# Performance work log

Hardware: AMD Instinct MI355X
Metric: run time of the kernel (lower is better)

Reference implementation:

```python
import jax, jax.numpy as jnp
import numpy as np

N = 1024      # num_nodes
D = 64        # node_embedding_dim
H = 64        # hidden_dim
LN_EPS = 1e-5


def setup_inputs() -> dict:
    key = jax.random.key(0)
    ks = jax.random.split(key, 6)
    node_embeddings = jax.random.normal(ks[0], (N, D), dtype=jnp.float32)
    valid_mask = jax.random.randint(ks[1], (N * N,), 0, 2).astype(jnp.float32)
    s1 = 1.0 / np.sqrt(2 * D)
    s2 = 1.0 / np.sqrt(H)
    W1 = jax.random.normal(ks[2], (2 * D, H), dtype=jnp.float32) * s1
    b1 = jnp.zeros((H,), jnp.float32)
    g1 = jnp.ones((H,), jnp.float32)
    be1 = jnp.zeros((H,), jnp.float32)
    W2 = jax.random.normal(ks[3], (H, H), dtype=jnp.float32) * s2
    b2 = jnp.zeros((H,), jnp.float32)
    g2 = jnp.ones((H,), jnp.float32)
    be2 = jnp.zeros((H,), jnp.float32)
    W3 = jax.random.normal(ks[4], (H, 1), dtype=jnp.float32) * s2
    b3 = jnp.zeros((1,), jnp.float32)
    return {
        "node_embeddings": node_embeddings, "valid_mask": valid_mask,
        "W1": W1, "b1": b1, "g1": g1, "be1": be1,
        "W2": W2, "b2": b2, "g2": g2, "be2": be2,
        "W3": W3, "b3": b3,
    }


def _layer_norm(x, g, b):
    m = jnp.mean(x, axis=-1, keepdims=True)
    v = jnp.mean((x - m) ** 2, axis=-1, keepdims=True)
    return (x - m) * jax.lax.rsqrt(v + LN_EPS) * g + b


def reference(node_embeddings, valid_mask, W1, b1, g1, be1, W2, b2, g2, be2, W3, b3):
    n, d = node_embeddings.shape
    # Build all ordered pairs (i, j): concat([emb_i, emb_j]) -> [n*n, 2d]
    src = jnp.broadcast_to(node_embeddings[:, None, :], (n, n, d))
    tgt = jnp.broadcast_to(node_embeddings[None, :, :], (n, n, d))
    e = jnp.concatenate([src, tgt], axis=-1).reshape(n * n, 2 * d)
    # MLP: Linear -> LayerNorm -> ReLU (x2 hidden) -> Linear(1)
    h = jax.nn.relu(_layer_norm(e @ W1 + b1, g1, be1))
    h = jax.nn.relu(_layer_norm(h @ W2 + b2, g2, be2))
    scores = (h @ W3 + b3)[:, 0]  # [n*n]
    # Original never scores self-edges (i == j) and multiplies by valid_mask.
    off_diag = 1.0 - jnp.eye(n, dtype=scores.dtype).reshape(-1)
    return scores * valid_mask * off_diag
```

## Files before the change

kernel.cpp:

```cpp
#include <hip/hip_runtime.h>
#include <hip/hip_bf16.h>

#define NN 1024
#define LN_EPS 1e-5f

typedef __bf16 bf16x8 __attribute__((ext_vector_type(8)));
typedef float floatx4 __attribute__((ext_vector_type(4)));
typedef float floatx2 __attribute__((ext_vector_type(2)));

__global__ void precompute_ab(const float* __restrict__ emb, const float* __restrict__ W1,
                              const float* __restrict__ b1, const float* __restrict__ W2,
                              float* __restrict__ Ap, float* __restrict__ Bt,
                              float* __restrict__ sumA, float* __restrict__ sumB,
                              __bf16* __restrict__ Wf) {
    if (blockIdx.x == 1024) {
        int lane = threadIdx.x;
        int m_l = lane & 15, kg = lane >> 4;
#pragma unroll
        for (int mt = 0; mt < 4; mt++)
#pragma unroll
            for (int kc = 0; kc < 2; kc++) {
                bf16x8 f;
#pragma unroll
                for (int t = 0; t < 8; t++) {
                    int k = kc * 32 + kg * 8 + t;
                    f[t] = (__bf16)W2[k * 64 + mt * 16 + m_l];
                }
                *(bf16x8*)&Wf[((mt * 2 + kc) * 64 + lane) * 8] = f;
            }
        return;
    }
    __shared__ __align__(16) float e[64];
    int i = blockIdx.x, h = threadIdx.x;
    e[h] = emb[i * 64 + h];
    __syncthreads();
    float a = b1[h], b = 0.f;
#pragma unroll
    for (int d = 0; d < 64; d++) {
        a = fmaf(e[d], W1[d * 64 + h], a);
        b = fmaf(e[d], W1[(64 + d) * 64 + h], b);
    }
    Ap[i * 64 + h] = a;
    Bt[h * NN + i] = b;
    float ra = a, rb = b;
#pragma unroll
    for (int off = 1; off < 64; off <<= 1) {
        ra += __shfl_xor(ra, off);
        rb += __shfl_xor(rb, off);
    }
    if (h == 0) { sumA[i] = ra; sumB[i] = rb; }
}

__global__ __launch_bounds__(256, 4) void fused(
    const float* __restrict__ Ap, const float* __restrict__ Bt, const __bf16* __restrict__ Wf,
    const float* __restrict__ sumA, const float* __restrict__ sumB,
    const float* __restrict__ g1, const float* __restrict__ be1, const float* __restrict__ b2,
    const float* __restrict__ g2, const float* __restrict__ be2, const float* __restrict__ W3,
    const float* __restrict__ b3, const float* __restrict__ mask, float* __restrict__ out) {
    __shared__ __align__(16) __bf16 h1t[4][64 * 64];

    int tid = threadIdx.x;
    int wave = tid >> 6, lane = tid & 63;
    int i = blockIdx.x >> 2;
    int j0 = (blockIdx.x & 3) * 256 + wave * 64;

    int m_l = lane & 15, kg = lane >> 4;
    const float* Arow = Ap + i * 64;

    float sBj = sumB[j0 + lane];
    const float* btp = Bt + j0 + lane;
    floatx2 x2[32];
    floatx2 qa = {0.f, 0.f}, qb = {0.f, 0.f};
#pragma unroll
    for (int h2 = 0; h2 < 32; h2++) {
        floatx2 bb = { btp[(2 * h2) * NN], btp[(2 * h2 + 1) * NN] };
        floatx2 aa = *(const floatx2*)&Arow[2 * h2];
        floatx2 v = aa + bb;
        x2[h2] = v;
        if (h2 & 1) qb += v * v;
        else        qa += v * v;
    }
    floatx2 qs = qa + qb;
    float sq = qs[0] + qs[1];
    float m1 = (sumA[i] + sBj) * 0.015625f;
    float rs1 = rsqrtf(fmaf(m1, -m1, sq * 0.015625f) + LN_EPS);
    floatx2 p1 = {rs1, rs1};
    float ofs = -m1 * rs1;
    floatx2 o1 = {ofs, ofs};

    bf16x8 afrag[4][2];
#pragma unroll
    for (int mt = 0; mt < 4; mt++)
#pragma unroll
        for (int kc = 0; kc < 2; kc++)
            afrag[mt][kc] = *(const bf16x8*)&Wf[((mt * 2 + kc) * 64 + lane) * 8];

    __bf16* rowp = &h1t[wave][lane * 64];
    int sw = lane & 7;
#pragma unroll
    for (int c = 0; c < 8; c++) {
        bf16x8 fr;
#pragma unroll
        for (int t = 0; t < 4; t++) {
            floatx2 gg = *(const floatx2*)&g1[c * 8 + 2 * t];
            floatx2 ee = *(const floatx2*)&be1[c * 8 + 2 * t];
            floatx2 xn = x2[c * 4 + t] * p1 + o1;
            floatx2 y  = xn * gg + ee;
            y = __builtin_elementwise_max(y, (floatx2){0.f, 0.f});
            fr[2 * t]     = (__bf16)y[0];
            fr[2 * t + 1] = (__bf16)y[1];
        }
        *(bf16x8*)(rowp + ((c ^ sw) * 8)) = fr;
    }
    asm volatile("s_waitcnt lgkmcnt(0)" ::: "memory");

    floatx4 b2r[4];
#pragma unroll
    for (int mt = 0; mt < 4; mt++) b2r[mt] = *(const floatx4*)&b2[mt * 16 + kg * 4];
    floatx4 acc[4][4];
#pragma unroll
    for (int mt = 0; mt < 4; mt++)
#pragma unroll
        for (int nt = 0; nt < 4; nt++) acc[mt][nt] = b2r[mt];

    const __bf16* wbase = &h1t[wave][0];
#pragma unroll
    for (int nt = 0; nt < 4; nt++) {
        int pair = nt * 16 + m_l;
#pragma unroll
        for (int kc = 0; kc < 2; kc++) {
            int chunk = kc * 4 + kg;
            bf16x8 bfrag = *(const bf16x8*)(wbase + pair * 64 + ((chunk ^ (pair & 7)) * 8));
#pragma unroll
            for (int mt = 0; mt < 4; mt++)
                acc[mt][nt] =
                    __builtin_amdgcn_mfma_f32_16x16x32_bf16(afrag[mt][kc], bfrag, acc[mt][nt], 0, 0, 0);
        }
    }

    floatx4 g2r[4], e2r[4], w3r[4];
#pragma unroll
    for (int mt = 0; mt < 4; mt++) {
        g2r[mt] = *(const floatx4*)&g2[mt * 16 + kg * 4];
        e2r[mt] = *(const floatx4*)&be2[mt * 16 + kg * 4];
        w3r[mt] = *(const floatx4*)&W3[mt * 16 + kg * 4];
    }
    float b3v = b3[0];

#pragma unroll
    for (int nt = 0; nt < 4; nt++) {
        floatx2 s2v = {0.f, 0.f}, q2v = {0.f, 0.f};
#pragma unroll
        for (int mt = 0; mt < 4; mt++) {
            floatx2 vlo = {acc[mt][nt][0], acc[mt][nt][1]};
            floatx2 vhi = {acc[mt][nt][2], acc[mt][nt][3]};
            s2v += vlo; s2v += vhi;
            q2v += vlo * vlo; q2v += vhi * vhi;
        }
        float s2 = s2v[0] + s2v[1];
        float q2 = q2v[0] + q2v[1];
        s2 += __shfl_xor(s2, 16); s2 += __shfl_xor(s2, 32);
        q2 += __shfl_xor(q2, 16); q2 += __shfl_xor(q2, 32);
        float m2 = s2 * 0.015625f;
        float rs2 = rsqrtf(fmaf(m2, -m2, q2 * 0.015625f) + LN_EPS);
        floatx2 P2 = {rs2, rs2};
        float o2s = -m2 * rs2;
        floatx2 O2 = {o2s, o2s};

        floatx2 scv = {0.f, 0.f};
#pragma unroll
        for (int mt = 0; mt < 4; mt++) {
#pragma unroll
            for (int hh = 0; hh < 2; hh++) {
                floatx2 v = {acc[mt][nt][2 * hh], acc[mt][nt][2 * hh + 1]};
                floatx2 g = {g2r[mt][2 * hh], g2r[mt][2 * hh + 1]};
                floatx2 e = {e2r[mt][2 * hh], e2r[mt][2 * hh + 1]};
                floatx2 w = {w3r[mt][2 * hh], w3r[mt][2 * hh + 1]};
                floatx2 y = (v * P2 + O2) * g + e;
                y = __builtin_elementwise_max(y, (floatx2){0.f, 0.f});
                scv += y * w;
            }
        }
        float sc = scv[0] + scv[1];
        sc += __shfl_xor(sc, 16); sc += __shfl_xor(sc, 32);

        if (kg == 0) {
            int j = j0 + nt * 16 + m_l;
            int p = i * NN + j;
            out[p] = (i == j) ? 0.f : (sc + b3v) * mask[p];
        }
    }
}

extern "C" void kernel_launch(void* const* d_in, const int* in_sizes, int n_in,
                              void* d_out, int out_size, void* d_ws, size_t ws_size,
                              hipStream_t stream) {
    const float* emb = (const float*)d_in[0];
    const float* mask = (const float*)d_in[1];
    const float* W1 = (const float*)d_in[2];
    const float* b1 = (const float*)d_in[3];
    const float* g1 = (const float*)d_in[4];
    const float* be1 = (const float*)d_in[5];
    const float* W2 = (const float*)d_in[6];
    const float* b2 = (const float*)d_in[7];
    const float* g2 = (const float*)d_in[8];
    const float* be2 = (const float*)d_in[9];
    const float* W3 = (const float*)d_in[10];
    const float* b3 = (const float*)d_in[11];
    float* out = (float*)d_out;

    float* Ap = (float*)d_ws;
    float* Bt = Ap + 65536;
    float* sA = Bt + 65536;
    float* sB = sA + 1024;
    __bf16* Wf = (__bf16*)(sB + 1024);

    precompute_ab<<<1025, 64, 0, stream>>>(emb, W1, b1, W2, Ap, Bt, sA, sB, Wf);
    fused<<<4096, 256, 0, stream>>>(Ap, Bt, Wf, sA, sB,
                                    g1, be1, b2, g2, be2, W3, b3, mask, out);
}
```

Measured before the change: 114.5 us.

## Compute LN1 variance via precomputed norms and dot product, row-major B

The first LayerNorm's sum of squares is now computed as |A_i|^2 + |B_j|^2 + 2·A_i·B_j, with both squared norms precomputed. This removes the need to hold the 64 summed activations in registers across the statistics pass. B is stored row-major instead of transposed, so each lane reads its own contiguous row with vector loads and reloads it when building the bf16 tile. The precompute kernel now handles 4 nodes per wave in 256-thread blocks. Expanding the square in fp32 risks cancellation error in the variance, and per-lane row reads are strided across lanes rather than coalesced.

```diff
diff --git a/kernel.cpp b/kernel.cpp
--- a/kernel.cpp
+++ b/kernel.cpp
@@ -8,13 +8,18 @@
 typedef float floatx4 __attribute__((ext_vector_type(4)));
 typedef float floatx2 __attribute__((ext_vector_type(2)));
 
-__global__ void precompute_ab(const float* __restrict__ emb, const float* __restrict__ W1,
-                              const float* __restrict__ b1, const float* __restrict__ W2,
-                              float* __restrict__ Ap, float* __restrict__ Bt,
-                              float* __restrict__ sumA, float* __restrict__ sumB,
-                              __bf16* __restrict__ Wf) {
-    if (blockIdx.x == 1024) {
-        int lane = threadIdx.x;
+__device__ __forceinline__ floatx4 splat4(float s) { return (floatx4){s, s, s, s}; }
+
+__global__ __launch_bounds__(256) void precompute_ab(
+    const float* __restrict__ emb, const float* __restrict__ W1,
+    const float* __restrict__ b1, const float* __restrict__ W2,
+    float* __restrict__ Ap, float* __restrict__ Bf,
+    float* __restrict__ sumA, float* __restrict__ sumB,
+    float* __restrict__ sumA2, float* __restrict__ sumB2,
+    __bf16* __restrict__ Wf) {
+    int tid = threadIdx.x, wv = tid >> 6, lane = tid & 63;
+    if (blockIdx.x == 64) {
+        if (wv != 0) return;
         int m_l = lane & 15, kg = lane >> 4;
 #pragma unroll
         for (int mt = 0; mt < 4; mt++)
@@ -30,30 +35,50 @@
             }
         return;
     }
-    __shared__ __align__(16) float e[64];
-    int i = blockIdx.x, h = threadIdx.x;
-    e[h] = emb[i * 64 + h];
-    __syncthreads();
-    float a = b1[h], b = 0.f;
-#pragma unroll
+    __shared__ __align__(16) float e[16][64];
+    int nb = blockIdx.x * 16 + wv * 4;
+#pragma unroll
+    for (int n = 0; n < 4; n++) e[wv * 4 + n][lane] = emb[(nb + n) * 64 + lane];
+    asm volatile("s_waitcnt vmcnt(0) lgkmcnt(0)" ::: "memory");
+
+    float b1l = b1[lane];
+    float a0 = b1l, a1 = b1l, a2 = b1l, a3 = b1l;
+    float c0 = 0.f, c1 = 0.f, c2 = 0.f, c3 = 0.f;
+    const float* w1a = W1 + lane;
+    const float* w1b = W1 + 64 * 64 + lane;
+#pragma unroll 16
     for (int d = 0; d < 64; d++) {
-        a = fmaf(e[d], W1[d * 64 + h], a);
-        b = fmaf(e[d], W1[(64 + d) * 64 + h], b);
-    }
-    Ap[i * 64 + h] = a;
-    Bt[h * NN + i] = b;
-    float ra = a, rb = b;
-#pragma unroll
-    for (int off = 1; off < 64; off <<= 1) {
-        ra += __shfl_xor(ra, off);
-        rb += __shfl_xor(rb, off);
-    }
-    if (h == 0) { sumA[i] = ra; sumB[i] = rb; }
+        float wa = w1a[d * 64];
+        float wb = w1b[d * 64];
+        float e0 = e[wv * 4 + 0][d], e1v = e[wv * 4 + 1][d];
+        float e2v = e[wv * 4 + 2][d], e3v = e[wv * 4 + 3][d];
+        a0 = fmaf(e0, wa, a0); a1 = fmaf(e1v, wa, a1);
+        a2 = fmaf(e2v, wa, a2); a3 = fmaf(e3v, wa, a3);
+        c0 = fmaf(e0, wb, c0); c1 = fmaf(e1v, wb, c1);
+        c2 = fmaf(e2v, wb, c2); c3 = fmaf(e3v, wb, c3);
+    }
+    float va[4] = {a0, a1, a2, a3}, vb[4] = {c0, c1, c2, c3};
+#pragma unroll
+    for (int n = 0; n < 4; n++) {
+        int node = nb + n;
+        Ap[node * 64 + lane] = va[n];
+        Bf[node * 64 + lane] = vb[n];
+        float ra = va[n], rb = vb[n], ra2 = va[n] * va[n], rb2 = vb[n] * vb[n];
+#pragma unroll
+        for (int off = 1; off < 64; off <<= 1) {
+            ra += __shfl_xor(ra, off);
+            rb += __shfl_xor(rb, off);
+            ra2 += __shfl_xor(ra2, off);
+            rb2 += __shfl_xor(rb2, off);
+        }
+        if (lane == 0) { sumA[node] = ra; sumB[node] = rb; sumA2[node] = ra2; sumB2[node] = rb2; }
+    }
 }
 
 __global__ __launch_bounds__(256, 4) void fused(
-    const float* __restrict__ Ap, const float* __restrict__ Bt, const __bf16* __restrict__ Wf,
+    const float* __restrict__ Ap, const float* __restrict__ Bf, const __bf16* __restrict__ Wf,
     const float* __restrict__ sumA, const float* __restrict__ sumB,
+    const float* __restrict__ sumA2, const float* __restrict__ sumB2,
     const float* __restrict__ g1, const float* __restrict__ be1, const float* __restrict__ b2,
     const float* __restrict__ g2, const float* __restrict__ be2, const float* __restrict__ W3,
     const float* __restrict__ b3, const float* __restrict__ mask, float* __restrict__ out) {
@@ -63,30 +88,24 @@
     int wave = tid >> 6, lane = tid & 63;
     int i = blockIdx.x >> 2;
     int j0 = (blockIdx.x & 3) * 256 + wave * 64;
+    int jme = j0 + lane;
 
     int m_l = lane & 15, kg = lane >> 4;
     const float* Arow = Ap + i * 64;
-
-    float sBj = sumB[j0 + lane];
-    const float* btp = Bt + j0 + lane;
-    floatx2 x2[32];
-    floatx2 qa = {0.f, 0.f}, qb = {0.f, 0.f};
-#pragma unroll
-    for (int h2 = 0; h2 < 32; h2++) {
-        floatx2 bb = { btp[(2 * h2) * NN], btp[(2 * h2 + 1) * NN] };
-        floatx2 aa = *(const floatx2*)&Arow[2 * h2];
-        floatx2 v = aa + bb;
-        x2[h2] = v;
-        if (h2 & 1) qb += v * v;
-        else        qa += v * v;
-    }
-    floatx2 qs = qa + qb;
-    float sq = qs[0] + qs[1];
-    float m1 = (sumA[i] + sBj) * 0.015625f;
+    const float* brow = Bf + jme * 64;
+
+    floatx4 dacc = splat4(0.f);
+#pragma unroll
+    for (int c = 0; c < 16; c++) {
+        floatx4 bb = *(const floatx4*)(brow + c * 4);
+        floatx4 aa = *(const floatx4*)&Arow[c * 4];
+        dacc = aa * bb + dacc;
+    }
+    float dot = (dacc[0] + dacc[1]) + (dacc[2] + dacc[3]);
+    float m1 = (sumA[i] + sumB[jme]) * 0.015625f;
+    float sq = fmaf(2.f, dot, sumA2[i] + sumB2[jme]);
     float rs1 = rsqrtf(fmaf(m1, -m1, sq * 0.015625f) + LN_EPS);
-    floatx2 p1 = {rs1, rs1};
-    float ofs = -m1 * rs1;
-    floatx2 o1 = {ofs, ofs};
+    floatx4 RS = splat4(rs1), OF = splat4(-m1 * rs1);
 
     bf16x8 afrag[4][2];
 #pragma unroll
@@ -99,17 +118,21 @@
     int sw = lane & 7;
 #pragma unroll
     for (int c = 0; c < 8; c++) {
+        floatx4 b0 = *(const floatx4*)(brow + c * 8);
+        floatx4 b1v = *(const floatx4*)(brow + c * 8 + 4);
+        floatx4 a0 = *(const floatx4*)&Arow[c * 8];
+        floatx4 a1 = *(const floatx4*)&Arow[c * 8 + 4];
+        floatx4 g0 = *(const floatx4*)&g1[c * 8];
+        floatx4 g1r = *(const floatx4*)&g1[c * 8 + 4];
+        floatx4 e0 = *(const floatx4*)&be1[c * 8];
+        floatx4 e1r = *(const floatx4*)&be1[c * 8 + 4];
+        floatx4 y0 = ((a0 + b0) * RS + OF) * g0 + e0;
+        floatx4 y1 = ((a1 + b1v) * RS + OF) * g1r + e1r;
+        y0 = __builtin_elementwise_max(y0, splat4(0.f));
+        y1 = __builtin_elementwise_max(y1, splat4(0.f));
         bf16x8 fr;
-#pragma unroll
-        for (int t = 0; t < 4; t++) {
-            floatx2 gg = *(const floatx2*)&g1[c * 8 + 2 * t];
-            floatx2 ee = *(const floatx2*)&be1[c * 8 + 2 * t];
-            floatx2 xn = x2[c * 4 + t] * p1 + o1;
-            floatx2 y  = xn * gg + ee;
-            y = __builtin_elementwise_max(y, (floatx2){0.f, 0.f});
-            fr[2 * t]     = (__bf16)y[0];
-            fr[2 * t + 1] = (__bf16)y[1];
-        }
+        fr[0] = (__bf16)y0[0]; fr[1] = (__bf16)y0[1]; fr[2] = (__bf16)y0[2]; fr[3] = (__bf16)y0[3];
+        fr[4] = (__bf16)y1[0]; fr[5] = (__bf16)y1[1]; fr[6] = (__bf16)y1[2]; fr[7] = (__bf16)y1[3];
         *(bf16x8*)(rowp + ((c ^ sw) * 8)) = fr;
     }
     asm volatile("s_waitcnt lgkmcnt(0)" ::: "memory");
@@ -210,12 +233,14 @@
     float* out = (float*)d_out;
 
     float* Ap = (float*)d_ws;
-    float* Bt = Ap + 65536;
-    float* sA = Bt + 65536;
+    float* Bf = Ap + 65536;
+    float* sA = Bf + 65536;
     float* sB = sA + 1024;
-    __bf16* Wf = (__bf16*)(sB + 1024);
-
-    precompute_ab<<<1025, 64, 0, stream>>>(emb, W1, b1, W2, Ap, Bt, sA, sB, Wf);
-    fused<<<4096, 256, 0, stream>>>(Ap, Bt, Wf, sA, sB,
+    float* sA2 = sB + 1024;
+    float* sB2 = sA2 + 1024;
+    __bf16* Wf = (__bf16*)(sB2 + 1024);
+
+    precompute_ab<<<65, 256, 0, stream>>>(emb, W1, b1, W2, Ap, Bf, sA, sB, sA2, sB2, Wf);
+    fused<<<4096, 256, 0, stream>>>(Ap, Bf, Wf, sA, sB, sA2, sB2,
                                     g1, be1, b2, g2, be2, W3, b3, mask, out);
 }
```

Result: slower. 146.3 us (+27.7%).

## Compute LN1 variance via pairwise dot GEMM and LN2 mean via weight column sums

Applied to the files above, without the earlier changes.

Expands the first LayerNorm's sum of squares as |a|^2 + |b|^2 + 2·a·b. The cross term comes from a new bf16 MFMA GEMM over all node pairs, so the fused kernel no longer holds 64 pre-LN values in registers for a first pass. The second LayerNorm's mean is now taken from h1 dotted with the row sums of W2 (plus the sum of b2), which removes the per-pair sum reduction after the MFMAs. This costs an extra kernel launch and a 4 MB dot matrix written to and read back from global memory. The bf16 dot product and the cancellation-prone variance formula may also reduce accuracy.

```diff
diff --git a/kernel.cpp b/kernel.cpp
--- a/kernel.cpp
+++ b/kernel.cpp
@@ -8,13 +8,19 @@
 typedef float floatx4 __attribute__((ext_vector_type(4)));
 typedef float floatx2 __attribute__((ext_vector_type(2)));
 
+__device__ __forceinline__ floatx4 splat4(float s) { return (floatx4){s, s, s, s}; }
+
 __global__ void precompute_ab(const float* __restrict__ emb, const float* __restrict__ W1,
                               const float* __restrict__ b1, const float* __restrict__ W2,
+                              const float* __restrict__ b2,
                               float* __restrict__ Ap, float* __restrict__ Bt,
+                              __bf16* __restrict__ Abf, __bf16* __restrict__ Bbf,
                               float* __restrict__ sumA, float* __restrict__ sumB,
+                              float* __restrict__ sumA2, float* __restrict__ sumB2,
+                              float* __restrict__ Wc, float* __restrict__ sb2,
                               __bf16* __restrict__ Wf) {
+    int lane = threadIdx.x;
     if (blockIdx.x == 1024) {
-        int lane = threadIdx.x;
         int m_l = lane & 15, kg = lane >> 4;
 #pragma unroll
         for (int mt = 0; mt < 4; mt++)
@@ -28,10 +34,17 @@
                 }
                 *(bf16x8*)&Wf[((mt * 2 + kc) * 64 + lane) * 8] = f;
             }
+        float s = 0.f;
+        for (int h = 0; h < 64; h++) s += W2[lane * 64 + h];
+        Wc[lane] = s;
+        float v = b2[lane];
+#pragma unroll
+        for (int off = 1; off < 64; off <<= 1) v += __shfl_xor(v, off);
+        if (lane == 0) sb2[0] = v;
         return;
     }
     __shared__ __align__(16) float e[64];
-    int i = blockIdx.x, h = threadIdx.x;
+    int i = blockIdx.x, h = lane;
     e[h] = emb[i * 64 + h];
     __syncthreads();
     float a = b1[h], b = 0.f;
@@ -42,18 +55,66 @@
     }
     Ap[i * 64 + h] = a;
     Bt[h * NN + i] = b;
-    float ra = a, rb = b;
+    Abf[i * 64 + h] = (__bf16)a;
+    Bbf[i * 64 + h] = (__bf16)b;
+    float ra = a, rb = b, ra2 = a * a, rb2 = b * b;
 #pragma unroll
     for (int off = 1; off < 64; off <<= 1) {
         ra += __shfl_xor(ra, off);
         rb += __shfl_xor(rb, off);
-    }
-    if (h == 0) { sumA[i] = ra; sumB[i] = rb; }
+        ra2 += __shfl_xor(ra2, off);
+        rb2 += __shfl_xor(rb2, off);
+    }
+    if (h == 0) { sumA[i] = ra; sumB[i] = rb; sumA2[i] = ra2; sumB2[i] = rb2; }
+}
+
+__global__ __launch_bounds__(256) void dotgemm(const __bf16* __restrict__ Abf,
+                                               const __bf16* __restrict__ Bbf,
+                                               float* __restrict__ dotM) {
+    int tid = threadIdx.x, wave = tid >> 6, lane = tid & 63;
+    int t = blockIdx.x * 4 + wave;
+    int ibase = (t >> 4) * 64, jbase = (t & 15) * 64;
+    int m_l = lane & 15, kg = lane >> 4;
+
+    floatx4 acc[4][4];
+#pragma unroll
+    for (int mt = 0; mt < 4; mt++)
+#pragma unroll
+        for (int nt = 0; nt < 4; nt++) acc[mt][nt] = splat4(0.f);
+
+#pragma unroll
+    for (int kc = 0; kc < 2; kc++) {
+        bf16x8 af[4], bf[4];
+#pragma unroll
+        for (int mt = 0; mt < 4; mt++)
+            af[mt] = *(const bf16x8*)&Abf[(ibase + mt * 16 + m_l) * 64 + kc * 32 + kg * 8];
+#pragma unroll
+        for (int nt = 0; nt < 4; nt++)
+            bf[nt] = *(const bf16x8*)&Bbf[(jbase + nt * 16 + m_l) * 64 + kc * 32 + kg * 8];
+#pragma unroll
+        for (int mt = 0; mt < 4; mt++)
+#pragma unroll
+            for (int nt = 0; nt < 4; nt++)
+                acc[mt][nt] = __builtin_amdgcn_mfma_f32_16x16x32_bf16(af[mt], bf[nt], acc[mt][nt], 0, 0, 0);
+    }
+#pragma unroll
+    for (int mt = 0; mt < 4; mt++)
+#pragma unroll
+        for (int nt = 0; nt < 4; nt++)
+#pragma unroll
+            for (int r = 0; r < 4; r++) {
+                int gi = ibase + mt * 16 + kg * 4 + r;
+                int gj = jbase + nt * 16 + m_l;
+                dotM[gi * NN + gj] = acc[mt][nt][r];
+            }
 }
 
 __global__ __launch_bounds__(256, 4) void fused(
     const float* __restrict__ Ap, const float* __restrict__ Bt, const __bf16* __restrict__ Wf,
+    const float* __restrict__ dotM,
     const float* __restrict__ sumA, const float* __restrict__ sumB,
+    const float* __restrict__ sumA2, const float* __restrict__ sumB2,
+    const float* __restrict__ Wcp, const float* __restrict__ sb2p,
     const float* __restrict__ g1, const float* __restrict__ be1, const float* __restrict__ b2,
     const float* __restrict__ g2, const float* __restrict__ be2, const float* __restrict__ W3,
     const float* __restrict__ b3, const float* __restrict__ mask, float* __restrict__ out) {
@@ -63,30 +124,19 @@
     int wave = tid >> 6, lane = tid & 63;
     int i = blockIdx.x >> 2;
     int j0 = (blockIdx.x & 3) * 256 + wave * 64;
+    int jme = j0 + lane;
 
     int m_l = lane & 15, kg = lane >> 4;
     const float* Arow = Ap + i * 64;
-
-    float sBj = sumB[j0 + lane];
-    const float* btp = Bt + j0 + lane;
-    floatx2 x2[32];
-    floatx2 qa = {0.f, 0.f}, qb = {0.f, 0.f};
-#pragma unroll
-    for (int h2 = 0; h2 < 32; h2++) {
-        floatx2 bb = { btp[(2 * h2) * NN], btp[(2 * h2 + 1) * NN] };
-        floatx2 aa = *(const floatx2*)&Arow[2 * h2];
-        floatx2 v = aa + bb;
-        x2[h2] = v;
-        if (h2 & 1) qb += v * v;
-        else        qa += v * v;
-    }
-    floatx2 qs = qa + qb;
-    float sq = qs[0] + qs[1];
-    float m1 = (sumA[i] + sBj) * 0.015625f;
+    const float* btp = Bt + jme;
+
+    float dot = dotM[i * NN + jme];
+    float m1 = (sumA[i] + sumB[jme]) * 0.015625f;
+    float sq = fmaf(2.f, dot, sumA2[i] + sumB2[jme]);
     float rs1 = rsqrtf(fmaf(m1, -m1, sq * 0.015625f) + LN_EPS);
-    floatx2 p1 = {rs1, rs1};
+    floatx2 P1 = {rs1, rs1};
     float ofs = -m1 * rs1;
-    floatx2 o1 = {ofs, ofs};
+    floatx2 O1 = {ofs, ofs};
 
     bf16x8 afrag[4][2];
 #pragma unroll
@@ -97,21 +147,27 @@
 
     __bf16* rowp = &h1t[wave][lane * 64];
     int sw = lane & 7;
+    floatx2 s2acc = {0.f, 0.f};
 #pragma unroll
     for (int c = 0; c < 8; c++) {
         bf16x8 fr;
 #pragma unroll
         for (int t = 0; t < 4; t++) {
-            floatx2 gg = *(const floatx2*)&g1[c * 8 + 2 * t];
-            floatx2 ee = *(const floatx2*)&be1[c * 8 + 2 * t];
-            floatx2 xn = x2[c * 4 + t] * p1 + o1;
-            floatx2 y  = xn * gg + ee;
+            int h = c * 8 + 2 * t;
+            floatx2 bb = { btp[h * NN], btp[(h + 1) * NN] };
+            floatx2 aa = *(const floatx2*)&Arow[h];
+            floatx2 gg = *(const floatx2*)&g1[h];
+            floatx2 ee = *(const floatx2*)&be1[h];
+            floatx2 wc = *(const floatx2*)&Wcp[h];
+            floatx2 y = ((aa + bb) * P1 + O1) * gg + ee;
             y = __builtin_elementwise_max(y, (floatx2){0.f, 0.f});
+            s2acc += y * wc;
             fr[2 * t]     = (__bf16)y[0];
             fr[2 * t + 1] = (__bf16)y[1];
         }
         *(bf16x8*)(rowp + ((c ^ sw) * 8)) = fr;
     }
+    float s2p = (s2acc[0] + s2acc[1]) + sb2p[0];
     asm volatile("s_waitcnt lgkmcnt(0)" ::: "memory");
 
     floatx4 b2r[4];
@@ -149,17 +205,16 @@
 
 #pragma unroll
     for (int nt = 0; nt < 4; nt++) {
-        floatx2 s2v = {0.f, 0.f}, q2v = {0.f, 0.f};
+        float s2 = __shfl(s2p, nt * 16 + m_l);
+        floatx2 q2v = {0.f, 0.f};
 #pragma unroll
         for (int mt = 0; mt < 4; mt++) {
             floatx2 vlo = {acc[mt][nt][0], acc[mt][nt][1]};
             floatx2 vhi = {acc[mt][nt][2], acc[mt][nt][3]};
-            s2v += vlo; s2v += vhi;
-            q2v += vlo * vlo; q2v += vhi * vhi;
-        }
-        float s2 = s2v[0] + s2v[1];
+            q2v += vlo * vlo;
+            q2v += vhi * vhi;
+        }
         float q2 = q2v[0] + q2v[1];
-        s2 += __shfl_xor(s2, 16); s2 += __shfl_xor(s2, 32);
         q2 += __shfl_xor(q2, 16); q2 += __shfl_xor(q2, 32);
         float m2 = s2 * 0.015625f;
         float rs2 = rsqrtf(fmaf(m2, -m2, q2 * 0.015625f) + LN_EPS);
@@ -213,9 +268,19 @@
     float* Bt = Ap + 65536;
     float* sA = Bt + 65536;
     float* sB = sA + 1024;
-    __bf16* Wf = (__bf16*)(sB + 1024);
-
-    precompute_ab<<<1025, 64, 0, stream>>>(emb, W1, b1, W2, Ap, Bt, sA, sB, Wf);
-    fused<<<4096, 256, 0, stream>>>(Ap, Bt, Wf, sA, sB,
+    float* sA2 = sB + 1024;
+    float* sB2 = sA2 + 1024;
+    float* Wc = sB2 + 1024;
+    float* sb2 = Wc + 64;
+    __bf16* Abf = (__bf16*)(sb2 + 64);
+    __bf16* Bbf = Abf + 65536;
+    __bf16* Wf = Bbf + 65536;
+    float* dotM = (float*)(Wf + 4096);
+    (void)ws_size;
+
+    precompute_ab<<<1025, 64, 0, stream>>>(emb, W1, b1, W2, b2, Ap, Bt, Abf, Bbf,
+                                           sA, sB, sA2, sB2, Wc, sb2, Wf);
+    dotgemm<<<64, 256, 0, stream>>>(Abf, Bbf, dotM);
+    fused<<<4096, 256, 0, stream>>>(Ap, Bt, Wf, dotM, sA, sB, sA2, sB2, Wc, sb2,
                                     g1, be1, b2, g2, be2, W3, b3, mask, out);
 }
```

Result: slower. 134.5 us (+17.4%).
